# Kernel optimization log

Measured on AMD Instinct MI355X. Metric: run time of the kernel, lower is better.

## Reference

```python
import jax, jax.numpy as jnp
import numpy as np

B, S, D, R = 256, 512, 128, 2048
H = 0.5  # integration step


def setup_inputs() -> dict:
    key = jax.random.key(0)
    ks = jax.random.split(key, 14)
    u = lambda k, shape, lo, hi: jax.random.uniform(k, shape, jnp.float32, lo, hi)
    bd, br = 1.0 / np.sqrt(D), 1.0 / np.sqrt(R)
    return {
        "inputs": jax.random.normal(ks[0], (B, S, D), jnp.float32),
        # input oscillator params (size D)
        "omega_in": u(ks[1], (D,), 1.0, 3.0),
        "gamma_in": u(ks[2], (D,), 0.1, 0.5),
        "alpha_in": u(ks[3], (D,), 0.5, 1.5),
        # input projection Linear(D -> R), torch layout [out, in]
        "W_proj": u(ks[4], (R, D), -bd, bd),
        "b_proj": u(ks[5], (R,), -bd, bd),
        # fixed reservoir oscillator params (size R)
        "omega_res": u(ks[6], (R,), 1.0, 3.0),
        "gamma_res": u(ks[7], (R,), 0.1, 0.5),
        "alpha_res": u(ks[8], (R,), 0.5, 1.5),
        # output oscillator params (size R)
        "omega_out": u(ks[9], (R,), 1.0, 3.0),
        "gamma_out": u(ks[10], (R,), 0.1, 0.5),
        "alpha_out": u(ks[11], (R,), 0.5, 1.5),
        # readout Linear(R -> D)
        "W_read": u(ks[12], (D, R), -br, br),
        "b_read": u(ks[13], (D,), -br, br),
    }


def _osc_step(f, x, y, omega, gamma, alpha):
    # x' = x + h*y ; y' = y + h*(alpha*f - 2|gamma|*y - |omega|^2 * x), clamped to [-5,5]
    accel = alpha * f - 2.0 * jnp.abs(gamma) * y - jnp.abs(omega) ** 2 * x
    x_new = jnp.clip(x + H * y, -5.0, 5.0)
    y_new = jnp.clip(y + H * accel, -5.0, 5.0)
    return x_new, y_new


def reference(inputs, omega_in, gamma_in, alpha_in, W_proj, b_proj,
              omega_res, gamma_res, alpha_res, omega_out, gamma_out, alpha_out,
              W_read, b_read):
    inputs_t = jnp.transpose(inputs, (1, 0, 2))  # [S, B, D]

    def step(carry, inp_t):
        x_in, y_in, x_res, y_res, x_out, y_out = carry
        x_in, y_in = _osc_step(inp_t, x_in, y_in, omega_in, gamma_in, alpha_in)
        proj = x_in @ W_proj.T + b_proj                      # [B, R]
        x_res, y_res = _osc_step(proj, x_res, y_res, omega_res, gamma_res, alpha_res)
        x_out, y_out = _osc_step(x_res, x_out, y_out, omega_out, gamma_out, alpha_out)
        pred = x_out @ W_read.T + b_read                     # [B, D]
        mse_out = jnp.mean((x_out - x_res) ** 2)             # scalar per step
        return (x_in, y_in, x_res, y_res, x_out, y_out), (pred, x_in, mse_out)

    z_d = jnp.zeros((B, D), inputs.dtype)
    z_r = jnp.zeros((B, R), inputs.dtype)
    carry0 = (z_d, z_d, z_r, z_r, z_r, z_r)
    _, (preds_t, x_in_seq, mse_out_seq) = jax.lax.scan(step, carry0, inputs_t)

    preds = jnp.transpose(preds_t, (1, 0, 2))  # [B, S, D]
    # pc_loss_in = sum_{t<S-1} mean((x_in(t) - inputs(t+1))^2)
    pc_loss_in = jnp.sum(jnp.mean((x_in_seq[:-1] - inputs_t[1:]) ** 2, axis=(1, 2)))
    pc_loss_out = jnp.sum(mse_out_seq)
    return preds, pc_loss_in, pc_loss_out
```

## Files before the change

### kernel.cpp

```cpp
#include <hip/hip_runtime.h>
#include <hip/hip_bf16.h>

#define Bn 256
#define Sn 512
#define Dn 128
#define Rn 2048
#define TB 32
#define NBLK (Sn / TB)
#define LDX 136
#define LDPs 1028
#define RG 1024

using bf16_t = __hip_bfloat16;
typedef short bf16x8 __attribute__((ext_vector_type(8)));
typedef float f32x4 __attribute__((ext_vector_type(4)));
typedef float f32x2 __attribute__((ext_vector_type(2)));

__device__ __forceinline__ f32x2 clip2(f32x2 v) {
  v = __builtin_elementwise_max(v, (f32x2)(-5.f));
  v = __builtin_elementwise_min(v, (f32x2)(5.f));
  return v;
}

__device__ __forceinline__ unsigned bf16rne(float f) {
  const unsigned u = __float_as_uint(f);
  return (u + 0x7fffu + ((u >> 16) & 1u)) >> 16;
}
__device__ __forceinline__ unsigned pack_bf16(f32x2 v) {
  return (bf16rne(v.y) << 16) | (bf16rne(v.x) & 0xffffu);
}

__global__ __launch_bounds__(256) void k_prep(const float* __restrict__ Wp,
                                              const float* __restrict__ Wr,
                                              bf16_t* __restrict__ Wp_b,
                                              bf16_t* __restrict__ Wr_b,
                                              float* __restrict__ losses) {
  const int i = blockIdx.x * 256 + threadIdx.x;
  Wp_b[i] = __float2bfloat16(Wp[i]);
  Wr_b[i] = __float2bfloat16(Wr[i]);
  if (i == 0) { losses[0] = 0.f; losses[1] = 0.f; }
}

__global__ __launch_bounds__(256) void k_zero(float* __restrict__ preds,
                                              const float* __restrict__ br) {
  const int i = blockIdx.x * 256 + threadIdx.x;
  const f32x4 bv = *(const f32x4*)(br + (i & 31) * 4);
  *((f32x4*)preds + i) = bv;
}

__global__ __launch_bounds__(512, 4) void k_fused(
    const float* __restrict__ inp,
    const float* __restrict__ om_i, const float* __restrict__ ga_i,
    const float* __restrict__ al_i,
    const bf16_t* __restrict__ Wp, const float* __restrict__ bp,
    const float* __restrict__ omr, const float* __restrict__ gar,
    const float* __restrict__ alr,
    const float* __restrict__ omo, const float* __restrict__ gao,
    const float* __restrict__ alo,
    const bf16_t* __restrict__ Wr,
    float* __restrict__ preds, float* __restrict__ losses) {
  __shared__ bf16_t Xs[TB * LDX];
  __shared__ bf16_t PX[TB * LDPs];
  __shared__ float smi[8], smo[8];

  const int tid = threadIdx.x;
  const int b = blockIdx.x & 255, g = blockIdx.x >> 8;
  const int rbase = g * RG;
  const int wv = tid >> 6, lane = tid & 63;
  const int lr = lane & 15, lq = lane >> 4;

  float xi = 0.f, yi = 0.f, pc_in = 0.f;
  float w2i = 0.f, g2i = 0.f, ai = 0.f;
  if (tid < Dn) {
    w2i = om_i[tid] * om_i[tid];
    g2i = 2.f * fabsf(ga_i[tid]);
    ai = al_i[tid];
  }
  const float* inpb = inp + (size_t)b * Sn * Dn;

  const int rl = tid * 2;
  f32x2 xr = (f32x2)0.f, yr = (f32x2)0.f, xo = (f32x2)0.f, yo = (f32x2)0.f;
  f32x2 w2r, g2r, arv, w2o, g2o, aov, bpv;
  {
    f32x2 t;
    t = *(const f32x2*)(omr + rbase + rl); w2r = t * t;
    t = *(const f32x2*)(gar + rbase + rl); g2r = __builtin_elementwise_abs(t) * 2.f;
    arv = *(const f32x2*)(alr + rbase + rl);
    t = *(const f32x2*)(omo + rbase + rl); w2o = t * t;
    t = *(const f32x2*)(gao + rbase + rl); g2o = __builtin_elementwise_abs(t) * 2.f;
    aov = *(const f32x2*)(alo + rbase + rl);
    bpv = *(const f32x2*)(bp + rbase + rl);
  }
  f32x2 pc_out2 = (f32x2)0.f;

  const bf16_t* wp_base = Wp + (size_t)(rbase + wv * 128 + lr) * Dn + lq * 8;
  const int d0 = wv * 16;
  const bf16_t* wr_base = Wr + (size_t)(d0 + lr) * Rn + rbase + lq * 8;

  auto phaseD = [&](int tp0) {
    f32x4 acc[2][2] = {{(f32x4)0.f, (f32x4)0.f}, {(f32x4)0.f, (f32x4)0.f}};
    bf16x8 bcur = *(const bf16x8*)(wr_base);
#pragma unroll 2
    for (int k0 = 0; k0 < RG; k0 += 32) {
      bf16x8 bnxt = bcur;
      if (k0 + 32 < RG) bnxt = *(const bf16x8*)(wr_base + k0 + 32);
      const int par = (k0 >> 5) & 1;
      bf16x8 a0 = *(const bf16x8*)&PX[(0 + lr) * LDPs + k0 + lq * 8];
      bf16x8 a1 = *(const bf16x8*)&PX[(16 + lr) * LDPs + k0 + lq * 8];
      acc[0][par] = __builtin_amdgcn_mfma_f32_16x16x32_bf16(a0, bcur, acc[0][par], 0, 0, 0);
      acc[1][par] = __builtin_amdgcn_mfma_f32_16x16x32_bf16(a1, bcur, acc[1][par], 0, 0, 0);
      bcur = bnxt;
    }
    float* outb = preds + (size_t)b * Sn * Dn + (size_t)tp0 * Dn;
#pragma unroll
    for (int i = 0; i < 2; ++i) {
      f32x4 s = acc[i][0] + acc[i][1];
#pragma unroll
      for (int r = 0; r < 4; ++r) {
        const int row = i * 16 + lq * 4 + r;
        atomicAdd(outb + (size_t)row * Dn + d0 + lr, s[r]);
      }
    }
  };

  for (int blk = 0; blk < NBLK; ++blk) {
    const int t0 = blk * TB;

    if (tid < Dn) {
#pragma unroll
      for (int tt = 0; tt < TB; ++tt) {
        const float f = inpb[(size_t)(t0 + tt) * Dn + tid];
        if (t0 + tt > 0) { const float e = xi - f; pc_in += e * e; }
        const float accel = ai * f - g2i * yi - w2i * xi;
        const float xn = fminf(fmaxf(xi + 0.5f * yi, -5.f), 5.f);
        const float yn = fminf(fmaxf(yi + 0.5f * accel, -5.f), 5.f);
        Xs[tt * LDX + tid] = __float2bfloat16(xn);
        xi = xn; yi = yn;
      }
    }
    if (blk > 0) phaseD(t0 - TB);
    __syncthreads();

    {
      bf16x8 af[2][4];
#pragma unroll
      for (int i = 0; i < 2; ++i)
#pragma unroll
        for (int k = 0; k < 4; ++k)
          af[i][k] = *(const bf16x8*)&Xs[(i * 16 + lr) * LDX + k * 32 + lq * 8];

      bf16x8 bfr[2][4];
#pragma unroll
      for (int k = 0; k < 4; ++k) {
        bfr[0][k] = *(const bf16x8*)(wp_base + (size_t)0 * 16 * Dn + k * 32);
        bfr[1][k] = *(const bf16x8*)(wp_base + (size_t)1 * 16 * Dn + k * 32);
      }
      for (int j = 0; j < 8; ++j) {
        const int pb = j & 1;
        f32x4 acc[2] = {(f32x4)0.f, (f32x4)0.f};
#pragma unroll
        for (int k = 0; k < 4; ++k) {
          acc[0] = __builtin_amdgcn_mfma_f32_16x16x32_bf16(af[0][k], bfr[pb][k], acc[0], 0, 0, 0);
          acc[1] = __builtin_amdgcn_mfma_f32_16x16x32_bf16(af[1][k], bfr[pb][k], acc[1], 0, 0, 0);
        }
        if (j + 2 < 8) {
#pragma unroll
          for (int k = 0; k < 4; ++k)
            bfr[pb][k] = *(const bf16x8*)(wp_base + (size_t)(j + 2) * 16 * Dn + k * 32);
        }
        const int cl = wv * 128 + j * 16 + lr;
#pragma unroll
        for (int i = 0; i < 2; ++i)
#pragma unroll
          for (int r = 0; r < 4; ++r)
            PX[(i * 16 + lq * 4 + r) * LDPs + cl] = __float2bfloat16(acc[i][r]);
      }
    }

    {
      unsigned pk = *(unsigned*)&PX[0 * LDPs + rl];
      for (int tt = 0; tt < TB; ++tt) {
        unsigned pk_n = pk;
        if (tt + 1 < TB) pk_n = *(unsigned*)&PX[(tt + 1) * LDPs + rl];
        f32x2 pv;
        pv.x = __uint_as_float(pk << 16);
        pv.y = __uint_as_float(pk & 0xffff0000u);
        pv += bpv;
        f32x2 acr = arv * pv - g2r * yr - w2r * xr;
        f32x2 xrn = clip2(xr + yr * 0.5f);
        f32x2 yrn = clip2(yr + acr * 0.5f);
        f32x2 aco = aov * xrn - g2o * yo - w2o * xo;
        f32x2 xon = clip2(xo + yo * 0.5f);
        f32x2 yon = clip2(yo + aco * 0.5f);
        f32x2 e = xon - xrn;
        pc_out2 += e * e;
        xr = xrn; yr = yrn; xo = xon; yo = yon;
        *(unsigned*)&PX[tt * LDPs + rl] = pack_bf16(xon);
        pk = pk_n;
      }
    }
    __syncthreads();
  }

  phaseD(Sn - TB);

  float vi = pc_in;
  float vo = pc_out2.x + pc_out2.y;
#pragma unroll
  for (int o = 32; o > 0; o >>= 1) {
    vi += __shfl_down(vi, o, 64);
    vo += __shfl_down(vo, o, 64);
  }
  if (lane == 0) { smi[wv] = vi; smo[wv] = vo; }
  __syncthreads();
  if (tid == 0) {
    float si = 0.f, so = 0.f;
#pragma unroll
    for (int w = 0; w < 8; ++w) { si += smi[w]; so += smo[w]; }
    if (g == 0) atomicAdd(losses + 0, si * (1.f / ((float)Bn * (float)Dn)));
    atomicAdd(losses + 1, so * (1.f / ((float)Bn * (float)Rn)));
  }
}

extern "C" void kernel_launch(void* const* d_in, const int* in_sizes, int n_in,
                              void* d_out, int out_size, void* d_ws, size_t ws_size,
                              hipStream_t stream) {
  const float* inputs    = (const float*)d_in[0];
  const float* omega_in  = (const float*)d_in[1];
  const float* gamma_in  = (const float*)d_in[2];
  const float* alpha_in  = (const float*)d_in[3];
  const float* W_proj    = (const float*)d_in[4];
  const float* b_proj    = (const float*)d_in[5];
  const float* omega_res = (const float*)d_in[6];
  const float* gamma_res = (const float*)d_in[7];
  const float* alpha_res = (const float*)d_in[8];
  const float* omega_out = (const float*)d_in[9];
  const float* gamma_out = (const float*)d_in[10];
  const float* alpha_out = (const float*)d_in[11];
  const float* W_read    = (const float*)d_in[12];
  const float* b_read    = (const float*)d_in[13];

  float* out = (float*)d_out;
  float* losses = out + (size_t)Bn * Sn * Dn;

  bf16_t* Wp_b = (bf16_t*)d_ws;
  bf16_t* Wr_b = Wp_b + (size_t)Rn * Dn;

  k_prep<<<1024, 256, 0, stream>>>(W_proj, W_read, Wp_b, Wr_b, losses);
  k_zero<<<(Bn * Sn * Dn / 4) / 256, 256, 0, stream>>>(out, b_read);
  k_fused<<<Bn * 2, 512, 0, stream>>>(inputs, omega_in, gamma_in, alpha_in,
                                      Wp_b, b_proj,
                                      omega_res, gamma_res, alpha_res,
                                      omega_out, gamma_out, alpha_out,
                                      Wr_b, out, losses);
}
```

Baseline: 699.6 us.

## Replace readout atomics with split partial buffers and a combine pass

Each of the two R-halves now writes its readout partial sums with plain nontemporal stores, one half to the output and the other to a workspace buffer. A separate combine kernel then adds the two buffers and the bias, taking the place of the zero-init kernel and the float atomicAdds. The readout K-loop is also restructured to keep four W_read fragments in flight as a deeper register prefetch. This trades atomic contention for an extra full-size read/write pass, and the split path only runs when the workspace is large enough.

```diff
diff --git a/kernel.cpp b/kernel.cpp
--- a/kernel.cpp
+++ b/kernel.cpp
@@ -48,6 +48,17 @@
   *((f32x4*)preds + i) = bv;
 }
 
+__global__ __launch_bounds__(256) void k_combine(float* __restrict__ out,
+                                                 const float* __restrict__ part,
+                                                 const float* __restrict__ br) {
+  const int i = blockIdx.x * 256 + threadIdx.x;
+  const f32x4 bv = *(const f32x4*)(br + (i & 31) * 4);
+  const f32x4 a = *((const f32x4*)out + i);
+  const f32x4 p = *((const f32x4*)part + i);
+  *((f32x4*)out + i) = a + p + bv;
+}
+
+template <int SPLIT>
 __global__ __launch_bounds__(512, 4) void k_fused(
     const float* __restrict__ inp,
     const float* __restrict__ om_i, const float* __restrict__ ga_i,
@@ -58,7 +69,8 @@
     const float* __restrict__ omo, const float* __restrict__ gao,
     const float* __restrict__ alo,
     const bf16_t* __restrict__ Wr,
-    float* __restrict__ preds, float* __restrict__ losses) {
+    float* __restrict__ preds, float* __restrict__ part,
+    float* __restrict__ losses) {
   __shared__ bf16_t Xs[TB * LDX];
   __shared__ bf16_t PX[TB * LDPs];
   __shared__ float smi[8], smo[8];
@@ -96,29 +108,42 @@
   const bf16_t* wp_base = Wp + (size_t)(rbase + wv * 128 + lr) * Dn + lq * 8;
   const int d0 = wv * 16;
   const bf16_t* wr_base = Wr + (size_t)(d0 + lr) * Rn + rbase + lq * 8;
+  float* pout = (SPLIT && g) ? part : preds;
 
   auto phaseD = [&](int tp0) {
     f32x4 acc[2][2] = {{(f32x4)0.f, (f32x4)0.f}, {(f32x4)0.f, (f32x4)0.f}};
-    bf16x8 bcur = *(const bf16x8*)(wr_base);
-#pragma unroll 2
-    for (int k0 = 0; k0 < RG; k0 += 32) {
-      bf16x8 bnxt = bcur;
-      if (k0 + 32 < RG) bnxt = *(const bf16x8*)(wr_base + k0 + 32);
-      const int par = (k0 >> 5) & 1;
-      bf16x8 a0 = *(const bf16x8*)&PX[(0 + lr) * LDPs + k0 + lq * 8];
-      bf16x8 a1 = *(const bf16x8*)&PX[(16 + lr) * LDPs + k0 + lq * 8];
-      acc[0][par] = __builtin_amdgcn_mfma_f32_16x16x32_bf16(a0, bcur, acc[0][par], 0, 0, 0);
-      acc[1][par] = __builtin_amdgcn_mfma_f32_16x16x32_bf16(a1, bcur, acc[1][par], 0, 0, 0);
-      bcur = bnxt;
-    }
-    float* outb = preds + (size_t)b * Sn * Dn + (size_t)tp0 * Dn;
+    bf16x8 bq0 = *(const bf16x8*)(wr_base + 0);
+    bf16x8 bq1 = *(const bf16x8*)(wr_base + 32);
+    bf16x8 bq2 = *(const bf16x8*)(wr_base + 64);
+    bf16x8 bq3 = *(const bf16x8*)(wr_base + 96);
+#define DSTEP(BQ, K0, PAR)                                                     \
+  {                                                                            \
+    bf16x8 a0 = *(const bf16x8*)&PX[(0 + lr) * LDPs + (K0) + lq * 8];          \
+    bf16x8 a1 = *(const bf16x8*)&PX[(16 + lr) * LDPs + (K0) + lq * 8];         \
+    acc[0][PAR] =                                                              \
+        __builtin_amdgcn_mfma_f32_16x16x32_bf16(a0, BQ, acc[0][PAR], 0, 0, 0); \
+    acc[1][PAR] =                                                              \
+        __builtin_amdgcn_mfma_f32_16x16x32_bf16(a1, BQ, acc[1][PAR], 0, 0, 0); \
+    if ((K0) + 128 < RG) BQ = *(const bf16x8*)(wr_base + (K0) + 128);          \
+  }
+    for (int k0 = 0; k0 < RG; k0 += 128) {
+      DSTEP(bq0, k0 + 0, 0)
+      DSTEP(bq1, k0 + 32, 1)
+      DSTEP(bq2, k0 + 64, 0)
+      DSTEP(bq3, k0 + 96, 1)
+    }
+#undef DSTEP
+    float* outb = pout + (size_t)b * Sn * Dn + (size_t)tp0 * Dn;
 #pragma unroll
     for (int i = 0; i < 2; ++i) {
       f32x4 s = acc[i][0] + acc[i][1];
 #pragma unroll
       for (int r = 0; r < 4; ++r) {
         const int row = i * 16 + lq * 4 + r;
-        atomicAdd(outb + (size_t)row * Dn + d0 + lr, s[r]);
+        if (SPLIT)
+          __builtin_nontemporal_store(s[r], outb + (size_t)row * Dn + d0 + lr);
+        else
+          atomicAdd(outb + (size_t)row * Dn + d0 + lr, s[r]);
       }
     }
   };
@@ -245,12 +270,26 @@
 
   bf16_t* Wp_b = (bf16_t*)d_ws;
   bf16_t* Wr_b = Wp_b + (size_t)Rn * Dn;
+  float* part = (float*)(Wr_b + (size_t)Rn * Dn);
+
+  const size_t need = 2u * Rn * Dn * sizeof(bf16_t) +
+                      (size_t)Bn * Sn * Dn * sizeof(float);
+  const bool split = ws_size >= need;
 
   k_prep<<<1024, 256, 0, stream>>>(W_proj, W_read, Wp_b, Wr_b, losses);
-  k_zero<<<(Bn * Sn * Dn / 4) / 256, 256, 0, stream>>>(out, b_read);
-  k_fused<<<Bn * 2, 512, 0, stream>>>(inputs, omega_in, gamma_in, alpha_in,
-                                      Wp_b, b_proj,
-                                      omega_res, gamma_res, alpha_res,
-                                      omega_out, gamma_out, alpha_out,
-                                      Wr_b, out, losses);
-}
+  if (split) {
+    k_fused<1><<<Bn * 2, 512, 0, stream>>>(inputs, omega_in, gamma_in, alpha_in,
+                                           Wp_b, b_proj,
+                                           omega_res, gamma_res, alpha_res,
+                                           omega_out, gamma_out, alpha_out,
+                                           Wr_b, out, part, losses);
+    k_combine<<<(Bn * Sn * Dn / 4) / 256, 256, 0, stream>>>(out, part, b_read);
+  } else {
+    k_zero<<<(Bn * Sn * Dn / 4) / 256, 256, 0, stream>>>(out, b_read);
+    k_fused<0><<<Bn * 2, 512, 0, stream>>>(inputs, omega_in, gamma_in, alpha_in,
+                                           Wp_b, b_proj,
+                                           omega_res, gamma_res, alpha_res,
+                                           omega_out, gamma_out, alpha_out,
+                                           Wr_b, out, part, losses);
+  }
+}
```

Result: no change. 698.9 us (-0.1%).
